# Performance work log

Measured on AMD Instinct MI355X. Metric: run time of the kernel, lower is better.

## Reference

```python
import jax, jax.numpy as jnp
import numpy as np

N_HEAD = 16
D_HEAD = 64
SCALE = 1.0 / D_HEAD ** 0.5


def setup_inputs() -> dict:
    key = jax.random.key(0)
    k1, k2, k3, k4 = jax.random.split(key, 4)
    bsz, qlen, d_embed, d_model = 4, 1024, 768, 1024
    return {
        "word_emb": jax.random.normal(k1, (bsz, qlen, d_embed), dtype=jnp.float32),
        "emb_w": jax.random.normal(k2, (d_embed, d_model), dtype=jnp.float32) * 0.02,
        "emb_b": jnp.zeros((d_model,), dtype=jnp.float32),
        "qkv_w0": jax.random.normal(k3, (d_model, 3 * N_HEAD * D_HEAD), dtype=jnp.float32) * 0.02,
        "qkv_w1": jax.random.normal(k4, (d_model, 3 * N_HEAD * D_HEAD), dtype=jnp.float32) * 0.02,
    }


def _mha(h, qkv_w):
    # h: [qlen, bsz, d_model]
    qlen, bsz, _ = h.shape
    heads = h @ qkv_w  # [qlen, bsz, 3*n_head*d_head]
    head_q, head_k, head_v = jnp.split(heads, 3, axis=-1)
    head_q = head_q.reshape(qlen, bsz, N_HEAD, D_HEAD)
    head_k = head_k.reshape(qlen, bsz, N_HEAD, D_HEAD)
    head_v = head_v.reshape(qlen, bsz, N_HEAD, D_HEAD)
    # explicit score materialization, faithful to the source einsum pattern
    attn_score = jnp.einsum('ibnd,jbnd->ijbn', head_q, head_k) * SCALE
    attn_prob = jax.nn.softmax(attn_score, axis=1)  # softmax over klen (dim=1)
    attn_vec = jnp.einsum('ijbn,jbnd->ibnd', attn_prob, head_v)
    attn_vec = attn_vec.reshape(qlen, bsz, N_HEAD * D_HEAD)
    return attn_vec, attn_prob


def reference(word_emb, emb_w, emb_b, qkv_w0, qkv_w1):
    # word_emb: [bsz, qlen, d_embed] -> [qlen, bsz, d_embed]
    h = jnp.transpose(word_emb, (1, 0, 2))
    h = h @ emb_w + emb_b  # emb_proj since d_embed != d_model
    # NOTE: the source computes pos_emb and word_emb + pos_emb, but then
    # overwrites with core_out = self.drop(word_emb), discarding pos_emb.
    # Dropout is identity in reference (eval) mode, so core_out == h.
    core_out = h
    core_out, attn_maps = _mha(core_out, qkv_w0)
    core_out, attn_maps = _mha(core_out, qkv_w1)
    return core_out, attn_maps
```

## Files before the change

kernel.cpp:

```cpp
#include <hip/hip_runtime.h>

#define LOG2E 1.44269504088896340736f

typedef __attribute__((ext_vector_type(8))) short short8;
typedef __attribute__((ext_vector_type(4))) float floatx4;

__device__ __forceinline__ float bf2f(short s) {
    union { float f; unsigned u; } v; v.u = ((unsigned)(unsigned short)s) << 16; return v.f;
}
__device__ __forceinline__ short f2bf(float f) {
    union { float f; unsigned u; } v; v.f = f;
    unsigned u = v.u;
    u += 0x7FFFu + ((u >> 16) & 1u);
    return (short)(u >> 16);
}

__global__ __launch_bounds__(256) void wcast(const float* __restrict__ W,
                                             short* __restrict__ Wt, int K, int N) {
    __shared__ float tile[64][65];
    int n0 = blockIdx.x * 64, k0 = blockIdx.y * 64;
    int t = threadIdx.x;
    int r = t >> 2, c4 = (t & 3) * 16;
    const float* src = W + (size_t)(k0 + r) * N + n0 + c4;
#pragma unroll
    for (int q = 0; q < 16; ++q) tile[r][c4 + q] = src[q];
    __syncthreads();
    short* dst = Wt + (size_t)(n0 + r) * K + k0 + c4;
    short8 o1, o2;
#pragma unroll
    for (int q = 0; q < 8; ++q) o1[q] = f2bf(tile[c4 + q][r]);
#pragma unroll
    for (int q = 0; q < 8; ++q) o2[q] = f2bf(tile[c4 + 8 + q][r]);
    *(short8*)(dst) = o1;
    *(short8*)(dst + 8) = o2;
}

__global__ __launch_bounds__(256) void a0cast(const float* __restrict__ we,
                                              short* __restrict__ A0) {
    int e = blockIdx.x * 256 + threadIdx.x;
    int m = e / 96, dc = (e % 96) * 8;
    int b = m & 3, s = m >> 2;
    const float* src = we + (size_t)(b * 1024 + s) * 768 + dc;
    short8 o;
#pragma unroll
    for (int q = 0; q < 8; ++q) o[q] = f2bf(src[q]);
    *(short8*)(A0 + (size_t)m * 768 + dc) = o;
}

__global__ __launch_bounds__(256) void gemm_bt(const short* __restrict__ A,
                                               const short* __restrict__ Bt,
                                               short* __restrict__ C,
                                               const float* __restrict__ bias,
                                               int K, int N) {
    __shared__ __align__(16) short sA[128 * 32];
    __shared__ __align__(16) short sB[128 * 32];
    int n0 = blockIdx.x * 128, m0 = blockIdx.y * 128;
    int tid = threadIdx.x;
    int lane = tid & 63, w = tid >> 6;
    int wm = (w >> 1) * 64, wn = (w & 1) * 64;
    int l15 = lane & 15, quad = lane >> 4;

    floatx4 zero = {0.f, 0.f, 0.f, 0.f};
    floatx4 acc[4][4];
#pragma unroll
    for (int i = 0; i < 4; ++i)
#pragma unroll
        for (int j = 0; j < 4; ++j) acc[i][j] = zero;

    for (int k0 = 0; k0 < K; k0 += 32) {
#pragma unroll
        for (int h = 0; h < 2; ++h) {
            int c = tid + h * 256;
            int row = c >> 2, off = (c & 3) * 8;
            *(short8*)(sA + row * 32 + off) =
                *(const short8*)(A + (size_t)(m0 + row) * K + k0 + off);
            *(short8*)(sB + row * 32 + off) =
                *(const short8*)(Bt + (size_t)(n0 + row) * K + k0 + off);
        }
        __syncthreads();
        short8 af[4], bfr[4];
#pragma unroll
        for (int i = 0; i < 4; ++i) {
            af[i]  = *(const short8*)(sA + (wm + i * 16 + l15) * 32 + quad * 8);
            bfr[i] = *(const short8*)(sB + (wn + i * 16 + l15) * 32 + quad * 8);
        }
#pragma unroll
        for (int i = 0; i < 4; ++i)
#pragma unroll
            for (int j = 0; j < 4; ++j)
                acc[i][j] = __builtin_amdgcn_mfma_f32_16x16x32_bf16(af[i], bfr[j], acc[i][j], 0, 0, 0);
        __syncthreads();
    }
#pragma unroll
    for (int i = 0; i < 4; ++i)
#pragma unroll
        for (int j = 0; j < 4; ++j) {
            int col = n0 + wn + j * 16 + l15;
            float bv = bias ? bias[col] : 0.f;
#pragma unroll
            for (int r = 0; r < 4; ++r) {
                int row = m0 + wm + i * 16 + quad * 4 + r;
                C[(size_t)row * N + col] = f2bf(acc[i][j][r] + bv);
            }
        }
}

__global__ __launch_bounds__(256) void pack_qkv(const short* __restrict__ heads,
                                                short* __restrict__ Qp,
                                                short* __restrict__ Kp,
                                                short* __restrict__ Vtp) {
    __shared__ short vt[64][72];
    int bn = blockIdx.y;
    int b = bn >> 4, n = bn & 15;
    int j0 = blockIdx.x * 64;
    int t = threadIdx.x;
#pragma unroll
    for (int h = 0; h < 2; ++h) {
        int c = t + h * 256;
        int jj = c >> 3, off = (c & 7) * 8;
        const short* base = heads + (size_t)((j0 + jj) * 4 + b) * 3072 + n * 64 + off;
        short8 qv = *(const short8*)(base);
        short8 kv = *(const short8*)(base + 1024);
        short8 vv = *(const short8*)(base + 2048);
        short8 qs;
#pragma unroll
        for (int e = 0; e < 8; ++e) qs[e] = f2bf(bf2f(qv[e]) * 0.125f);
        *(short8*)(Qp + (size_t)bn * 65536 + (j0 + jj) * 64 + off) = qs;
        *(short8*)(Kp + (size_t)bn * 65536 + (j0 + jj) * 64 + off) = kv;
#pragma unroll
        for (int e = 0; e < 8; ++e) vt[jj][off + e] = vv[e];
    }
    __syncthreads();
#pragma unroll
    for (int h = 0; h < 2; ++h) {
        int c = t + h * 256;
        int d = c >> 3, joff = (c & 7) * 8;
        short8 o;
#pragma unroll
        for (int e = 0; e < 8; ++e) o[e] = vt[joff + e][d];
        *(short8*)(Vtp + (size_t)bn * 65536 + d * 1024 + j0 + joff) = o;
    }
}

template <bool L2>
__global__ __launch_bounds__(64) void fattn(const short* __restrict__ Qp,
                                            const short* __restrict__ Kp,
                                            const short* __restrict__ Vtp,
                                            void* __restrict__ Optr,
                                            float* __restrict__ linv) {
    __shared__ __align__(16) short plds[16 * 32];
    int bn = blockIdx.y, b = bn >> 4, n = bn & 15;
    int i0 = blockIdx.x * 16;
    int lane = threadIdx.x, l15 = lane & 15, quad = lane >> 4;
    const short* Qb = Qp + (size_t)bn * 65536;
    const short* Kb = Kp + (size_t)bn * 65536;
    const short* Vb = Vtp + (size_t)bn * 65536;

    short8 qf0 = *(const short8*)(Qb + (i0 + l15) * 64 + quad * 8);
    short8 qf1 = *(const short8*)(Qb + (i0 + l15) * 64 + 32 + quad * 8);

    floatx4 zero = {0.f, 0.f, 0.f, 0.f};
    floatx4 o[4] = {zero, zero, zero, zero};
    float lsum[4] = {0.f, 0.f, 0.f, 0.f};

    for (int j0 = 0; j0 < 1024; j0 += 32) {
        floatx4 p[2];
#pragma unroll
        for (int jh = 0; jh < 2; ++jh) {
            const short* kr = Kb + (j0 + jh * 16 + l15) * 64 + quad * 8;
            short8 kf0 = *(const short8*)(kr);
            short8 kf1 = *(const short8*)(kr + 32);
            floatx4 s = zero;
            s = __builtin_amdgcn_mfma_f32_16x16x32_bf16(qf0, kf0, s, 0, 0, 0);
            s = __builtin_amdgcn_mfma_f32_16x16x32_bf16(qf1, kf1, s, 0, 0, 0);
#pragma unroll
            for (int r = 0; r < 4; ++r) p[jh][r] = __builtin_amdgcn_exp2f(s[r] * LOG2E);
        }
        float rs[4];
#pragma unroll
        for (int r = 0; r < 4; ++r) rs[r] = p[0][r] + p[1][r];
#pragma unroll
        for (int off = 1; off < 16; off <<= 1)
#pragma unroll
            for (int r = 0; r < 4; ++r) rs[r] += __shfl_xor(rs[r], off);
#pragma unroll
        for (int r = 0; r < 4; ++r) lsum[r] += rs[r];
#pragma unroll
        for (int jh = 0; jh < 2; ++jh)
#pragma unroll
            for (int r = 0; r < 4; ++r)
                plds[(quad * 4 + r) * 32 + jh * 16 + l15] = f2bf(p[jh][r]);
        __syncthreads();
        short8 pa = *(const short8*)(plds + l15 * 32 + quad * 8);
#pragma unroll
        for (int tt = 0; tt < 4; ++tt) {
            short8 vf = *(const short8*)(Vb + (tt * 16 + l15) * 1024 + j0 + quad * 8);
            o[tt] = __builtin_amdgcn_mfma_f32_16x16x32_bf16(pa, vf, o[tt], 0, 0, 0);
        }
        __syncthreads();
    }
    float rn[4];
#pragma unroll
    for (int r = 0; r < 4; ++r) rn[r] = 1.f / lsum[r];
#pragma unroll
    for (int tt = 0; tt < 4; ++tt)
#pragma unroll
        for (int r = 0; r < 4; ++r) {
            float val = o[tt][r] * rn[r];
            int row = i0 + quad * 4 + r;
            int col = n * 64 + tt * 16 + l15;
            size_t idx = (size_t)(row * 4 + b) * 1024 + col;
            if (L2) ((float*)Optr)[idx] = val;
            else    ((short*)Optr)[idx] = f2bf(val);
        }
    if (L2 && l15 == 0) {
#pragma unroll
        for (int r = 0; r < 4; ++r) linv[bn * 1024 + i0 + quad * 4 + r] = rn[r];
    }
}

__global__ __launch_bounds__(256) void pfin(const short* __restrict__ Qp,
                                            const short* __restrict__ Kp,
                                            const float* __restrict__ linv,
                                            float* __restrict__ Pout) {
    __shared__ short sP[64 * 512];
    int j0 = blockIdx.x * 32, i0 = blockIdx.y * 16;
    int tid = threadIdx.x, wv = tid >> 6, lane = tid & 63;
    int l15 = lane & 15, quad = lane >> 4;
    floatx4 zero = {0.f, 0.f, 0.f, 0.f};
    for (int bi = 0; bi < 16; ++bi) {
        int bn = wv * 16 + bi;
        const short* Qb = Qp + (size_t)bn * 65536;
        const short* Kb = Kp + (size_t)bn * 65536;
        short8 qf0 = *(const short8*)(Qb + (i0 + l15) * 64 + quad * 8);
        short8 qf1 = *(const short8*)(Qb + (i0 + l15) * 64 + 32 + quad * 8);
        float li[4];
#pragma unroll
        for (int r = 0; r < 4; ++r) li[r] = linv[bn * 1024 + i0 + quad * 4 + r];
#pragma unroll
        for (int jh = 0; jh < 2; ++jh) {
            const short* kr = Kb + (j0 + jh * 16 + l15) * 64 + quad * 8;
            short8 kf0 = *(const short8*)(kr);
            short8 kf1 = *(const short8*)(kr + 32);
            floatx4 s = zero;
            s = __builtin_amdgcn_mfma_f32_16x16x32_bf16(qf0, kf0, s, 0, 0, 0);
            s = __builtin_amdgcn_mfma_f32_16x16x32_bf16(qf1, kf1, s, 0, 0, 0);
#pragma unroll
            for (int r = 0; r < 4; ++r)
                sP[bn * 512 + (quad * 4 + r) * 32 + jh * 16 + l15] =
                    f2bf(__builtin_amdgcn_exp2f(s[r] * LOG2E) * li[r]);
        }
    }
    __syncthreads();
    int ii = tid >> 4, q = tid & 15;
    float* dst = Pout + (size_t)(i0 + ii) * 65536 + j0 * 64 + q * 128;
#pragma unroll
    for (int e4 = 0; e4 < 32; ++e4) {
        int pos = q * 128 + e4 * 4;
        int jj = pos >> 6, bnb = pos & 63;
        float4 v;
        v.x = bf2f(sP[(bnb + 0) * 512 + ii * 32 + jj]);
        v.y = bf2f(sP[(bnb + 1) * 512 + ii * 32 + jj]);
        v.z = bf2f(sP[(bnb + 2) * 512 + ii * 32 + jj]);
        v.w = bf2f(sP[(bnb + 3) * 512 + ii * 32 + jj]);
        *(float4*)(dst + e4 * 4) = v;
    }
}

extern "C" void kernel_launch(void* const* d_in, const int* in_sizes, int n_in,
                              void* d_out, int out_size, void* d_ws, size_t ws_size,
                              hipStream_t stream) {
    const float* word_emb = (const float*)d_in[0];
    const float* emb_w    = (const float*)d_in[1];
    const float* emb_b    = (const float*)d_in[2];
    const float* qkv_w0   = (const float*)d_in[3];
    const float* qkv_w1   = (const float*)d_in[4];
    float* out0 = (float*)d_out;
    float* out1 = out0 + 4194304;

    char* ws = (char*)d_ws;
    short* A0    = (short*)(ws);
    short* WtE   = (short*)(ws + 6291456);
    short* Wt0   = (short*)(ws + 7864320);
    short* Wt1   = (short*)(ws + 14155776);
    short* hbuf  = (short*)(ws + 20447232);
    short* h2    = (short*)(ws + 28835840);
    short* heads = (short*)(ws + 37224448);
    short* Qp    = (short*)(ws + 62390272);
    short* Kp    = (short*)(ws + 70778880);
    short* Vtp   = (short*)(ws + 79167488);
    float* linv  = (float*)(ws + 87556096);

    wcast<<<dim3(16, 12), 256, 0, stream>>>(emb_w, WtE, 768, 1024);
    wcast<<<dim3(48, 16), 256, 0, stream>>>(qkv_w0, Wt0, 1024, 3072);
    wcast<<<dim3(48, 16), 256, 0, stream>>>(qkv_w1, Wt1, 1024, 3072);
    a0cast<<<1536, 256, 0, stream>>>(word_emb, A0);

    gemm_bt<<<dim3(8, 32), 256, 0, stream>>>(A0, WtE, hbuf, emb_b, 768, 1024);
    gemm_bt<<<dim3(24, 32), 256, 0, stream>>>(hbuf, Wt0, heads, nullptr, 1024, 3072);
    pack_qkv<<<dim3(16, 64), 256, 0, stream>>>(heads, Qp, Kp, Vtp);
    fattn<false><<<dim3(64, 64), 64, 0, stream>>>(Qp, Kp, Vtp, (void*)h2, nullptr);
    gemm_bt<<<dim3(24, 32), 256, 0, stream>>>(h2, Wt1, heads, nullptr, 1024, 3072);
    pack_qkv<<<dim3(16, 64), 256, 0, stream>>>(heads, Qp, Kp, Vtp);
    fattn<true><<<dim3(64, 64), 64, 0, stream>>>(Qp, Kp, Vtp, (void*)out0, linv);
    pfin<<<dim3(32, 64), 256, 0, stream>>>(Qp, Kp, linv, out1);
}
```

Measured before the change: 783.3 us.

## Double query rows per attention block, transpose score MFMA, use direct global-to-LDS loads

The attention kernel now handles 32 query rows per wavefront instead of 16, so each K and V fragment loaded from global memory feeds two MFMA tiles. Swapping the MFMA operand order computes S transposed, which lets each lane sum probabilities locally and write packed 4-element vectors to LDS instead of doing per-step cross-lane shuffles. The GEMM stages tiles through LDS with global_load_lds instead of going through registers. The trade-off is half as many attention blocks and more registers per lane, which may lower occupancy.

```diff
diff --git a/kernel.cpp b/kernel.cpp
--- a/kernel.cpp
+++ b/kernel.cpp
@@ -3,6 +3,7 @@
 #define LOG2E 1.44269504088896340736f
 
 typedef __attribute__((ext_vector_type(8))) short short8;
+typedef __attribute__((ext_vector_type(4))) short short4v;
 typedef __attribute__((ext_vector_type(4))) float floatx4;
 
 __device__ __forceinline__ float bf2f(short s) {
@@ -13,6 +14,11 @@
     unsigned u = v.u;
     u += 0x7FFFu + ((u >> 16) & 1u);
     return (short)(u >> 16);
+}
+
+__device__ __forceinline__ void gl_lds16(const void* g, void* l) {
+    __builtin_amdgcn_global_load_lds((const __attribute__((address_space(1))) void*)g,
+                                     (__attribute__((address_space(3))) void*)l, 16, 0, 0);
 }
 
 __global__ __launch_bounds__(256) void wcast(const float* __restrict__ W,
@@ -59,6 +65,7 @@
     int lane = tid & 63, w = tid >> 6;
     int wm = (w >> 1) * 64, wn = (w & 1) * 64;
     int l15 = lane & 15, quad = lane >> 4;
+    int srow = lane >> 2, scoff = (lane & 3) * 8;
 
     floatx4 zero = {0.f, 0.f, 0.f, 0.f};
     floatx4 acc[4][4];
@@ -70,12 +77,10 @@
     for (int k0 = 0; k0 < K; k0 += 32) {
 #pragma unroll
         for (int h = 0; h < 2; ++h) {
-            int c = tid + h * 256;
-            int row = c >> 2, off = (c & 3) * 8;
-            *(short8*)(sA + row * 32 + off) =
-                *(const short8*)(A + (size_t)(m0 + row) * K + k0 + off);
-            *(short8*)(sB + row * 32 + off) =
-                *(const short8*)(Bt + (size_t)(n0 + row) * K + k0 + off);
+            int seg = w * 2 + h;
+            int row = seg * 16 + srow;
+            gl_lds16(A + (size_t)(m0 + row) * K + k0 + scoff, sA + seg * 512);
+            gl_lds16(Bt + (size_t)(n0 + row) * K + k0 + scoff, sB + seg * 512);
         }
         __syncthreads();
         short8 af[4], bfr[4];
@@ -148,75 +153,95 @@
                                             const short* __restrict__ Vtp,
                                             void* __restrict__ Optr,
                                             float* __restrict__ linv) {
-    __shared__ __align__(16) short plds[16 * 32];
+    __shared__ __align__(16) short plds[32 * 32];
     int bn = blockIdx.y, b = bn >> 4, n = bn & 15;
-    int i0 = blockIdx.x * 16;
+    int i0 = blockIdx.x * 32;
     int lane = threadIdx.x, l15 = lane & 15, quad = lane >> 4;
     const short* Qb = Qp + (size_t)bn * 65536;
     const short* Kb = Kp + (size_t)bn * 65536;
     const short* Vb = Vtp + (size_t)bn * 65536;
 
-    short8 qf0 = *(const short8*)(Qb + (i0 + l15) * 64 + quad * 8);
-    short8 qf1 = *(const short8*)(Qb + (i0 + l15) * 64 + 32 + quad * 8);
-
+    short8 qf[2][2];
+#pragma unroll
+    for (int ib = 0; ib < 2; ++ib) {
+        qf[ib][0] = *(const short8*)(Qb + (i0 + ib * 16 + l15) * 64 + quad * 8);
+        qf[ib][1] = *(const short8*)(Qb + (i0 + ib * 16 + l15) * 64 + 32 + quad * 8);
+    }
     floatx4 zero = {0.f, 0.f, 0.f, 0.f};
-    floatx4 o[4] = {zero, zero, zero, zero};
-    float lsum[4] = {0.f, 0.f, 0.f, 0.f};
+    floatx4 o[2][4];
+#pragma unroll
+    for (int ib = 0; ib < 2; ++ib)
+#pragma unroll
+        for (int tt = 0; tt < 4; ++tt) o[ib][tt] = zero;
+    float lsum[2] = {0.f, 0.f};
 
     for (int j0 = 0; j0 < 1024; j0 += 32) {
-        floatx4 p[2];
-#pragma unroll
-        for (int jh = 0; jh < 2; ++jh) {
-            const short* kr = Kb + (j0 + jh * 16 + l15) * 64 + quad * 8;
+#pragma unroll
+        for (int jb = 0; jb < 2; ++jb) {
+            const short* kr = Kb + (j0 + jb * 16 + l15) * 64 + quad * 8;
             short8 kf0 = *(const short8*)(kr);
             short8 kf1 = *(const short8*)(kr + 32);
-            floatx4 s = zero;
-            s = __builtin_amdgcn_mfma_f32_16x16x32_bf16(qf0, kf0, s, 0, 0, 0);
-            s = __builtin_amdgcn_mfma_f32_16x16x32_bf16(qf1, kf1, s, 0, 0, 0);
-#pragma unroll
-            for (int r = 0; r < 4; ++r) p[jh][r] = __builtin_amdgcn_exp2f(s[r] * LOG2E);
-        }
-        float rs[4];
-#pragma unroll
-        for (int r = 0; r < 4; ++r) rs[r] = p[0][r] + p[1][r];
-#pragma unroll
-        for (int off = 1; off < 16; off <<= 1)
-#pragma unroll
-            for (int r = 0; r < 4; ++r) rs[r] += __shfl_xor(rs[r], off);
-#pragma unroll
-        for (int r = 0; r < 4; ++r) lsum[r] += rs[r];
-#pragma unroll
-        for (int jh = 0; jh < 2; ++jh)
-#pragma unroll
-            for (int r = 0; r < 4; ++r)
-                plds[(quad * 4 + r) * 32 + jh * 16 + l15] = f2bf(p[jh][r]);
+#pragma unroll
+            for (int ib = 0; ib < 2; ++ib) {
+                floatx4 s = zero;
+                s = __builtin_amdgcn_mfma_f32_16x16x32_bf16(kf0, qf[ib][0], s, 0, 0, 0);
+                s = __builtin_amdgcn_mfma_f32_16x16x32_bf16(kf1, qf[ib][1], s, 0, 0, 0);
+                short4v pk;
+                float ls = 0.f;
+#pragma unroll
+                for (int r = 0; r < 4; ++r) {
+                    float p = __builtin_amdgcn_exp2f(s[r] * LOG2E);
+                    ls += p;
+                    pk[r] = f2bf(p);
+                }
+                lsum[ib] += ls;
+                *(short4v*)(plds + (ib * 16 + l15) * 32 + jb * 16 + quad * 4) = pk;
+            }
+        }
         __syncthreads();
-        short8 pa = *(const short8*)(plds + l15 * 32 + quad * 8);
+        short8 pa[2];
+        pa[0] = *(const short8*)(plds + l15 * 32 + quad * 8);
+        pa[1] = *(const short8*)(plds + (16 + l15) * 32 + quad * 8);
 #pragma unroll
         for (int tt = 0; tt < 4; ++tt) {
             short8 vf = *(const short8*)(Vb + (tt * 16 + l15) * 1024 + j0 + quad * 8);
-            o[tt] = __builtin_amdgcn_mfma_f32_16x16x32_bf16(pa, vf, o[tt], 0, 0, 0);
+#pragma unroll
+            for (int ib = 0; ib < 2; ++ib)
+                o[ib][tt] = __builtin_amdgcn_mfma_f32_16x16x32_bf16(pa[ib], vf, o[ib][tt], 0, 0, 0);
         }
         __syncthreads();
     }
-    float rn[4];
-#pragma unroll
-    for (int r = 0; r < 4; ++r) rn[r] = 1.f / lsum[r];
-#pragma unroll
-    for (int tt = 0; tt < 4; ++tt)
-#pragma unroll
-        for (int r = 0; r < 4; ++r) {
-            float val = o[tt][r] * rn[r];
-            int row = i0 + quad * 4 + r;
-            int col = n * 64 + tt * 16 + l15;
-            size_t idx = (size_t)(row * 4 + b) * 1024 + col;
-            if (L2) ((float*)Optr)[idx] = val;
-            else    ((short*)Optr)[idx] = f2bf(val);
-        }
-    if (L2 && l15 == 0) {
-#pragma unroll
-        for (int r = 0; r < 4; ++r) linv[bn * 1024 + i0 + quad * 4 + r] = rn[r];
-    }
+    float rinv[2];
+#pragma unroll
+    for (int ib = 0; ib < 2; ++ib) {
+        float t = lsum[ib];
+        t += __shfl_xor(t, 16);
+        t += __shfl_xor(t, 32);
+        rinv[ib] = 1.f / t;
+    }
+    if (L2 && quad == 0) {
+        linv[bn * 1024 + i0 + l15] = rinv[0];
+        linv[bn * 1024 + i0 + 16 + l15] = rinv[1];
+    }
+    float rn[2][4];
+#pragma unroll
+    for (int ib = 0; ib < 2; ++ib)
+#pragma unroll
+        for (int r = 0; r < 4; ++r)
+            rn[ib][r] = __shfl(rinv[ib], quad * 4 + r);
+#pragma unroll
+    for (int ib = 0; ib < 2; ++ib)
+#pragma unroll
+        for (int tt = 0; tt < 4; ++tt)
+#pragma unroll
+            for (int r = 0; r < 4; ++r) {
+                float val = o[ib][tt][r] * rn[ib][r];
+                int row = i0 + ib * 16 + quad * 4 + r;
+                int col = n * 64 + tt * 16 + l15;
+                size_t idx = (size_t)(row * 4 + b) * 1024 + col;
+                if (L2) ((float*)Optr)[idx] = val;
+                else    ((short*)Optr)[idx] = f2bf(val);
+            }
 }
 
 __global__ __launch_bounds__(256) void pfin(const short* __restrict__ Qp,
@@ -234,21 +259,20 @@
         const short* Kb = Kp + (size_t)bn * 65536;
         short8 qf0 = *(const short8*)(Qb + (i0 + l15) * 64 + quad * 8);
         short8 qf1 = *(const short8*)(Qb + (i0 + l15) * 64 + 32 + quad * 8);
-        float li[4];
-#pragma unroll
-        for (int r = 0; r < 4; ++r) li[r] = linv[bn * 1024 + i0 + quad * 4 + r];
-#pragma unroll
-        for (int jh = 0; jh < 2; ++jh) {
-            const short* kr = Kb + (j0 + jh * 16 + l15) * 64 + quad * 8;
+        float li = linv[bn * 1024 + i0 + l15];
+#pragma unroll
+        for (int jb = 0; jb < 2; ++jb) {
+            const short* kr = Kb + (j0 + jb * 16 + l15) * 64 + quad * 8;
             short8 kf0 = *(const short8*)(kr);
             short8 kf1 = *(const short8*)(kr + 32);
             floatx4 s = zero;
-            s = __builtin_amdgcn_mfma_f32_16x16x32_bf16(qf0, kf0, s, 0, 0, 0);
-            s = __builtin_amdgcn_mfma_f32_16x16x32_bf16(qf1, kf1, s, 0, 0, 0);
+            s = __builtin_amdgcn_mfma_f32_16x16x32_bf16(kf0, qf0, s, 0, 0, 0);
+            s = __builtin_amdgcn_mfma_f32_16x16x32_bf16(kf1, qf1, s, 0, 0, 0);
+            short4v pk;
 #pragma unroll
             for (int r = 0; r < 4; ++r)
-                sP[bn * 512 + (quad * 4 + r) * 32 + jh * 16 + l15] =
-                    f2bf(__builtin_amdgcn_exp2f(s[r] * LOG2E) * li[r]);
+                pk[r] = f2bf(__builtin_amdgcn_exp2f(s[r] * LOG2E) * li);
+            *(short4v*)(sP + bn * 512 + l15 * 32 + jb * 16 + quad * 4) = pk;
         }
     }
     __syncthreads();
@@ -299,9 +323,9 @@
     gemm_bt<<<dim3(8, 32), 256, 0, stream>>>(A0, WtE, hbuf, emb_b, 768, 1024);
     gemm_bt<<<dim3(24, 32), 256, 0, stream>>>(hbuf, Wt0, heads, nullptr, 1024, 3072);
     pack_qkv<<<dim3(16, 64), 256, 0, stream>>>(heads, Qp, Kp, Vtp);
-    fattn<false><<<dim3(64, 64), 64, 0, stream>>>(Qp, Kp, Vtp, (void*)h2, nullptr);
+    fattn<false><<<dim3(32, 64), 64, 0, stream>>>(Qp, Kp, Vtp, (void*)h2, nullptr);
     gemm_bt<<<dim3(24, 32), 256, 0, stream>>>(h2, Wt1, heads, nullptr, 1024, 3072);
     pack_qkv<<<dim3(16, 64), 256, 0, stream>>>(heads, Qp, Kp, Vtp);
-    fattn<true><<<dim3(64, 64), 64, 0, stream>>>(Qp, Kp, Vtp, (void*)out0, linv);
+    fattn<true><<<dim3(32, 64), 64, 0, stream>>>(Qp, Kp, Vtp, (void*)out0, linv);
     pfin<<<dim3(32, 64), 256, 0, stream>>>(Qp, Kp, linv, out1);
 }
```

New measurement: 686.2 us. -12.4%, faster.
